# Kernel optimization log

Hardware: AMD Instinct MI355X
Metric: run time of the kernel (lower is better)

The kernel has to match this reference:

```python
import jax, jax.numpy as jnp
import numpy as np

S_GRID = 14.0
L_COORD = 5.0
L_NOOBJ = 0.5
B = 2


def _xywh2xyxy(b):
    # b: [..., 4] with (x, y, w, h); x,y are divided by S per the original module
    xy = b[..., :2] / S_GRID
    wh = b[..., 2:4]
    return jnp.concatenate([xy - 0.5 * wh, xy + 0.5 * wh], axis=-1)


def setup_inputs() -> dict:
    key = jax.random.key(0)
    k1, k2, k3, k4 = jax.random.split(key, 4)
    N, S, C = 4096, 14, 20
    pred_tensor = jax.random.uniform(k1, (N, S, S, B * 5 + C), dtype=jnp.float32, minval=0.05, maxval=1.0)
    target_boxes = jax.random.uniform(k2, (N, S, S, 4), dtype=jnp.float32, minval=0.05, maxval=1.0)
    target_cls = jax.random.normal(k3, (N, S, S, C), dtype=jnp.float32)
    has_object_map = jax.random.randint(k4, (N, S, S), 0, 2).astype(jnp.bool_)
    return {"pred_tensor": pred_tensor, "target_boxes": target_boxes,
            "target_cls": target_cls, "has_object_map": has_object_map}


def reference(pred_tensor, target_boxes, target_cls, has_object_map):
    N = pred_tensor.shape[0]
    mask = has_object_map                      # [N,S,S] bool
    maskf = mask.astype(pred_tensor.dtype)
    pb = pred_tensor[..., :B * 5].reshape(*pred_tensor.shape[:3], B, 5)  # [N,S,S,B,5]
    pc = pred_tensor[..., B * 5:]              # [N,S,S,20]

    # class loss: masked sum of squared errors over classes
    cls_loss = jnp.sum(maskf * jnp.sum((target_cls - pc) ** 2, axis=-1))

    # no-object loss: conf^2 on cells without objects, summed over both boxes
    conf = pb[..., 4]                          # [N,S,S,B]
    no_obj_loss = L_NOOBJ * jnp.sum(jnp.where(~mask[..., None], conf, 0.0) ** 2)

    # per-cell IoU of target vs each of the B predicted boxes (diag of original NxM)
    t_xyxy = _xywh2xyxy(target_boxes)          # [N,S,S,4]
    p_xyxy = _xywh2xyxy(pb[..., :4])           # [N,S,S,B,4]
    lt = jnp.maximum(t_xyxy[..., None, :2], p_xyxy[..., :2])
    rb = jnp.minimum(t_xyxy[..., None, 2:], p_xyxy[..., 2:])
    wh = jnp.clip(rb - lt, 0.0)
    inter = wh[..., 0] * wh[..., 1]            # [N,S,S,B]
    area_t = (t_xyxy[..., 2] - t_xyxy[..., 0]) * (t_xyxy[..., 3] - t_xyxy[..., 1])
    area_p = (p_xyxy[..., 2] - p_xyxy[..., 0]) * (p_xyxy[..., 3] - p_xyxy[..., 1])
    iou = inter / (area_t[..., None] + area_p - inter)  # [N,S,S,B]

    best_iou = jnp.max(iou, axis=-1)           # [N,S,S]
    best_idx = jnp.argmax(iou, axis=-1)        # [N,S,S]
    best_box = jnp.take_along_axis(pb, best_idx[..., None, None], axis=3)[..., 0, :]  # [N,S,S,5]

    xy_diff = jnp.where(mask[..., None], best_box[..., :2] - target_boxes[..., :2], 0.0)
    wh_p = jnp.where(mask[..., None], best_box[..., 2:4], 1.0)
    wh_t = jnp.where(mask[..., None], target_boxes[..., 2:4], 1.0)
    reg_loss = L_COORD * (jnp.sum(xy_diff ** 2)
                          + jnp.sum((jnp.sqrt(wh_p) - jnp.sqrt(wh_t)) ** 2))

    # containing-object confidence loss: mse(best_iou, best_box_conf) on object cells
    containing_obj_loss = jnp.sum(jnp.where(mask, best_iou - best_box[..., 4], 0.0) ** 2)

    total_loss = (cls_loss + no_obj_loss + reg_loss + containing_obj_loss) / N
    return (total_loss, reg_loss, containing_obj_loss, no_obj_loss, cls_loss)
```

## Files before the change

kernel.cpp:

```cpp
#include <hip/hip_runtime.h>
#include <math.h>


#define BLOCK 256
#define WPB 4
#define CPW 64

typedef __attribute__((address_space(3))) void       lds_void_t;
typedef __attribute__((address_space(1))) const void gbl_void_t;

__global__ __launch_bounds__(BLOCK, 4) void k_yolo(
    const float*  __restrict__ pred,
    const float4* __restrict__ tbox4,
    const float4* __restrict__ tcls4,
    const int*    __restrict__ mask,
    float4*       __restrict__ partial,
    int n_cells)
{
    __shared__ float  sp[WPB][CPW * 30];
    __shared__ float4 swr[WPB];
    const int tid  = threadIdx.x;
    const int lane = tid & 63;
    const int w    = tid >> 6;
    const long long nc    = n_cells;
    const long long cell0 = ((long long)blockIdx.x * WPB + w) * CPW;
    const long long base  = (cell0 < nc) ? cell0 : (nc - CPW);
    const int remc = (int)(((nc - base) < CPW) ? (nc - base) : CPW);
    const int lim5 = remc * 5;
    const int li   = (lane < remc) ? lane : (remc - 1);

    const char* gb   = (const char*)pred + base * 120;
    const char* gend = (const char*)pred + nc * 120 - 16;
    char* lb = (char*)&sp[w][0];
    #pragma unroll
    for (int i = 0; i < 7; ++i) {
        const char* ga = gb + i * 1024 + lane * 16;
        if (ga > gend) ga = gend;
        __builtin_amdgcn_global_load_lds((gbl_void_t*)ga,
                                         (lds_void_t*)(lb + i * 1024), 16, 0, 0);
    }
    if (lane < 32) {
        const char* ga = gb + 7168 + lane * 16;
        if (ga > gend) ga = gend;
        __builtin_amdgcn_global_load_lds((gbl_void_t*)ga,
                                         (lds_void_t*)(lb + 7168), 16, 0, 0);
    }

    int    mraw = mask[base + li];
    float4 tb   = tbox4[base + li];
    const float4* t4 = tcls4 + base * 5;
    float4 t[5];
    #pragma unroll
    for (int i = 0; i < 5; ++i) {
        int j  = lane + i * 64;
        int jc = (j < lim5) ? j : (lim5 - 1);
        t[i] = t4[jc];
    }

    __builtin_amdgcn_s_waitcnt(0xF70);
    __asm__ volatile("" ::: "memory");

    const bool  vf    = (cell0 + (long long)lane) < nc;
    const int   mflag = vf ? mraw : 0;
    const float mff   = (float)mflag;
    const float vff   = vf ? 1.0f : 0.0f;
    const unsigned long long mbits = __ballot(mflag != 0);

    float cls = 0.f, noobj, reg, cont;
    {
        const float2* pc2 = reinterpret_cast<const float2*>(sp[w] + lane * 30);
        float2 v0 = pc2[0], v1 = pc2[1], v2 = pc2[2], v3 = pc2[3], v4 = pc2[4];
        float txc = tb.x / 14.0f, tyc = tb.y / 14.0f;
        float t0 = txc - 0.5f * tb.z, t1 = tyc - 0.5f * tb.w;
        float t2 = txc + 0.5f * tb.z, t3 = tyc + 0.5f * tb.w;
        float area_t = (t2 - t0) * (t3 - t1);
        float bx[2] = { v0.x, v2.y }, by[2] = { v0.y, v3.x };
        float bw[2] = { v1.x, v3.y }, bh[2] = { v1.y, v4.x };
        float bcf[2] = { v2.x, v4.y };
        float iou[2];
        #pragma unroll
        for (int b = 0; b < 2; ++b) {
            float px = bx[b] / 14.0f, py = by[b] / 14.0f;
            float q0 = px - 0.5f * bw[b], q1 = py - 0.5f * bh[b];
            float q2 = px + 0.5f * bw[b], q3 = py + 0.5f * bh[b];
            float lt0 = fmaxf(t0, q0), lt1 = fmaxf(t1, q1);
            float rb0 = fminf(t2, q2), rb1 = fminf(t3, q3);
            float ww = fmaxf(rb0 - lt0, 0.f), hh = fmaxf(rb1 - lt1, 0.f);
            float inter = ww * hh;
            float area_p = (q2 - q0) * (q3 - q1);
            iou[b] = inter / (area_t + area_p - inter);
        }
        int bi = (iou[1] > iou[0]) ? 1 : 0;
        float dx = bx[bi] - tb.x, dy = by[bi] - tb.y;
        float swd = sqrtf(bw[bi]) - sqrtf(tb.z);
        float shd = sqrtf(bh[bi]) - sqrtf(tb.w);
        reg  = mff * 5.0f * (dx*dx + dy*dy + swd*swd + shd*shd);
        float dco = iou[bi] - bcf[bi];
        cont = mff * dco * dco;
        noobj = (vff - mff) * 0.5f * (v2.x * v2.x + v4.y * v4.y);
    }

    #pragma unroll
    for (int i = 0; i < 5; ++i) {
        int j = lane + i * 64;
        int c = j / 5;
        int q = j - 5 * c;
        float mcf = (float)((int)((mbits >> c) & 1ull));
        mcf = (j < lim5) ? mcf : 0.0f;
        const float2* s2 = reinterpret_cast<const float2*>(sp[w] + c * 30 + 10 + q * 4);
        float2 a = s2[0], b2 = s2[1];
        float d0 = t[i].x - a.x,  d1 = t[i].y - a.y;
        float d2 = t[i].z - b2.x, d3 = t[i].w - b2.y;
        cls += mcf * (d0*d0 + d1*d1 + d2*d2 + d3*d3);
    }

    #pragma unroll
    for (int off = 32; off; off >>= 1) {
        cls   += __shfl_down(cls,   off, 64);
        noobj += __shfl_down(noobj, off, 64);
        reg   += __shfl_down(reg,   off, 64);
        cont  += __shfl_down(cont,  off, 64);
    }
    if (lane == 0) swr[w] = make_float4(cls, noobj, reg, cont);
    __syncthreads();
    if (tid == 0) {
        float4 a = swr[0];
        #pragma unroll
        for (int i = 1; i < WPB; ++i) {
            float4 b = swr[i];
            a.x += b.x; a.y += b.y; a.z += b.z; a.w += b.w;
        }
        partial[blockIdx.x] = a;
    }
}

__global__ __launch_bounds__(BLOCK) void k_final(
    const float4* __restrict__ partial, int nblocks,
    float* __restrict__ out, float invN)
{
    float4 acc = make_float4(0.f, 0.f, 0.f, 0.f);
    for (int b = threadIdx.x; b < nblocks; b += BLOCK) {
        float4 v = partial[b];
        acc.x += v.x; acc.y += v.y; acc.z += v.z; acc.w += v.w;
    }
    #pragma unroll
    for (int off = 32; off; off >>= 1) {
        acc.x += __shfl_down(acc.x, off, 64);
        acc.y += __shfl_down(acc.y, off, 64);
        acc.z += __shfl_down(acc.z, off, 64);
        acc.w += __shfl_down(acc.w, off, 64);
    }
    __shared__ float4 sw[WPB];
    int lane = threadIdx.x & 63, w = threadIdx.x >> 6;
    if (lane == 0) sw[w] = acc;
    __syncthreads();
    if (threadIdx.x == 0) {
        float cls = 0.f, noobj = 0.f, reg = 0.f, cont = 0.f;
        #pragma unroll
        for (int i = 0; i < WPB; ++i) {
            cls += sw[i].x; noobj += sw[i].y; reg += sw[i].z; cont += sw[i].w;
        }
        out[0] = (cls + noobj + reg + cont) * invN;
        out[1] = reg;
        out[2] = cont;
        out[3] = noobj;
        out[4] = cls;
    }
}

extern "C" void kernel_launch(void* const* d_in, const int* in_sizes, int n_in,
                              void* d_out, int out_size, void* d_ws, size_t ws_size,
                              hipStream_t stream) {
    const float*  pred  = (const float*)d_in[0];
    const float4* tbox4 = (const float4*)d_in[1];
    const float4* tcls4 = (const float4*)d_in[2];
    const int*    mask  = (const int*)d_in[3];
    float* out = (float*)d_out;
    float4* partial = (float4*)d_ws;

    int n_cells = in_sizes[3];
    int N = in_sizes[0] / (14 * 14 * 30);
    int nblocks = (n_cells + BLOCK - 1) / BLOCK;

    hipLaunchKernelGGL(k_yolo, dim3(nblocks), dim3(BLOCK), 0, stream,
                       pred, tbox4, tcls4, mask, partial, n_cells);
    hipLaunchKernelGGL(k_final, dim3(1), dim3(BLOCK), 0, stream,
                       partial, nblocks, out, 1.0f / (float)N);
}
```

Baseline: 203.3 us.

## Process four tiles per wave with software-pipelined LDS prefetch of next tile

Each wave now loops over four 64-cell tiles instead of one, reading the current tile's prediction data from LDS into registers, then issuing the async global-to-LDS load and register loads for the next tile before computing on the current one. The aim is to overlap memory latency with compute and cut the block count and partial-sum work by a factor of four. Class-target loads use nontemporal hints. In exchange, register pressure rises from double-buffered contexts, fewer blocks are in flight, and the launch-bounds occupancy hint was dropped.

```diff
diff --git a/kernel.cpp b/kernel.cpp
--- a/kernel.cpp
+++ b/kernel.cpp
@@ -5,78 +5,98 @@
 #define BLOCK 256
 #define WPB 4
 #define CPW 64
+#define TPW 4
 
 typedef __attribute__((address_space(3))) void       lds_void_t;
 typedef __attribute__((address_space(1))) const void gbl_void_t;
-
-__global__ __launch_bounds__(BLOCK, 4) void k_yolo(
-    const float*  __restrict__ pred,
-    const float4* __restrict__ tbox4,
-    const float4* __restrict__ tcls4,
-    const int*    __restrict__ mask,
-    float4*       __restrict__ partial,
-    int n_cells)
-{
-    __shared__ float  sp[WPB][CPW * 30];
-    __shared__ float4 swr[WPB];
-    const int tid  = threadIdx.x;
-    const int lane = tid & 63;
-    const int w    = tid >> 6;
-    const long long nc    = n_cells;
-    const long long cell0 = ((long long)blockIdx.x * WPB + w) * CPW;
-    const long long base  = (cell0 < nc) ? cell0 : (nc - CPW);
-    const int remc = (int)(((nc - base) < CPW) ? (nc - base) : CPW);
-    const int lim5 = remc * 5;
-    const int li   = (lane < remc) ? lane : (remc - 1);
-
-    const char* gb   = (const char*)pred + base * 120;
+typedef float vf4 __attribute__((ext_vector_type(4)));
+
+struct TileCtx {
+    long long cell0;
+    int       lim5;
+    int       mraw;
+    vf4       tb;
+    vf4       t[5];
+};
+
+__device__ __forceinline__ void issue_tile(
+    long long tile, long long ntiles, long long nc, int lane,
+    const float* __restrict__ pred, const vf4* __restrict__ tbox4,
+    const vf4* __restrict__ tcls4, const int* __restrict__ mask,
+    char* lb, TileCtx& cx)
+{
+    cx.cell0 = tile * CPW;
+    long long tt = (tile < ntiles) ? tile : (ntiles - 1);
+    long long b  = tt * CPW;
+    b = (b + CPW <= nc) ? b : (nc - CPW);
+    int remc = (int)(((nc - b) < (long long)CPW) ? (nc - b) : CPW);
+    cx.lim5 = remc * 5;
+    int li = (lane < remc) ? lane : (remc - 1);
+
+    const char* gb   = (const char*)pred + b * 120;
     const char* gend = (const char*)pred + nc * 120 - 16;
-    char* lb = (char*)&sp[w][0];
     #pragma unroll
     for (int i = 0; i < 7; ++i) {
-        const char* ga = gb + i * 1024 + lane * 16;
+        const char* ga = gb + i * 1024 + (long long)lane * 16;
         if (ga > gend) ga = gend;
         __builtin_amdgcn_global_load_lds((gbl_void_t*)ga,
                                          (lds_void_t*)(lb + i * 1024), 16, 0, 0);
     }
     if (lane < 32) {
-        const char* ga = gb + 7168 + lane * 16;
+        const char* ga = gb + 7168 + (long long)lane * 16;
         if (ga > gend) ga = gend;
         __builtin_amdgcn_global_load_lds((gbl_void_t*)ga,
                                          (lds_void_t*)(lb + 7168), 16, 0, 0);
     }
-
-    int    mraw = mask[base + li];
-    float4 tb   = tbox4[base + li];
-    const float4* t4 = tcls4 + base * 5;
-    float4 t[5];
+    cx.mraw = mask[b + li];
+    cx.tb   = tbox4[b + li];
+    const vf4* t4 = tcls4 + b * 5;
     #pragma unroll
     for (int i = 0; i < 5; ++i) {
         int j  = lane + i * 64;
-        int jc = (j < lim5) ? j : (lim5 - 1);
-        t[i] = t4[jc];
-    }
-
-    __builtin_amdgcn_s_waitcnt(0xF70);
-    __asm__ volatile("" ::: "memory");
-
-    const bool  vf    = (cell0 + (long long)lane) < nc;
-    const int   mflag = vf ? mraw : 0;
+        int jc = (j < cx.lim5) ? j : (cx.lim5 - 1);
+        cx.t[i] = __builtin_nontemporal_load(&t4[jc]);
+    }
+}
+
+__device__ __forceinline__ void read_pred(
+    const float* spw, int lane,
+    float2 (&v)[5], float2 (&pa)[5], float2 (&pb)[5])
+{
+    const float2* pc2 = reinterpret_cast<const float2*>(spw + lane * 30);
+    #pragma unroll
+    for (int i = 0; i < 5; ++i) v[i] = pc2[i];
+    #pragma unroll
+    for (int i = 0; i < 5; ++i) {
+        int j = lane + i * 64;
+        int c = j / 5;
+        int q = j - 5 * c;
+        const float2* s2 = reinterpret_cast<const float2*>(spw + c * 30 + 10 + q * 4);
+        pa[i] = s2[0];
+        pb[i] = s2[1];
+    }
+}
+
+__device__ __forceinline__ void compute_tile(
+    int lane, long long nc, const TileCtx& cx,
+    const float2 (&v)[5], const float2 (&pa)[5], const float2 (&pb)[5],
+    float& cls, float& noobj, float& reg, float& cont)
+{
+    const bool  vfb   = (cx.cell0 + (long long)lane) < nc;
+    const int   mflag = vfb ? cx.mraw : 0;
     const float mff   = (float)mflag;
-    const float vff   = vf ? 1.0f : 0.0f;
+    const float vff   = vfb ? 1.0f : 0.0f;
     const unsigned long long mbits = __ballot(mflag != 0);
 
-    float cls = 0.f, noobj, reg, cont;
     {
-        const float2* pc2 = reinterpret_cast<const float2*>(sp[w] + lane * 30);
-        float2 v0 = pc2[0], v1 = pc2[1], v2 = pc2[2], v3 = pc2[3], v4 = pc2[4];
+        vf4 tb = cx.tb;
         float txc = tb.x / 14.0f, tyc = tb.y / 14.0f;
         float t0 = txc - 0.5f * tb.z, t1 = tyc - 0.5f * tb.w;
         float t2 = txc + 0.5f * tb.z, t3 = tyc + 0.5f * tb.w;
         float area_t = (t2 - t0) * (t3 - t1);
-        float bx[2] = { v0.x, v2.y }, by[2] = { v0.y, v3.x };
-        float bw[2] = { v1.x, v3.y }, bh[2] = { v1.y, v4.x };
-        float bcf[2] = { v2.x, v4.y };
+        float bx[2] = { v[0].x, v[2].y }, by[2] = { v[0].y, v[3].x };
+        float bw[2] = { v[1].x, v[3].y }, bh[2] = { v[1].y, v[4].x };
+        float bcf[2] = { v[2].x, v[4].y };
         float iou[2];
         #pragma unroll
         for (int b = 0; b < 2; ++b) {
@@ -94,24 +114,63 @@
         float dx = bx[bi] - tb.x, dy = by[bi] - tb.y;
         float swd = sqrtf(bw[bi]) - sqrtf(tb.z);
         float shd = sqrtf(bh[bi]) - sqrtf(tb.w);
-        reg  = mff * 5.0f * (dx*dx + dy*dy + swd*swd + shd*shd);
+        reg  += mff * 5.0f * (dx*dx + dy*dy + swd*swd + shd*shd);
         float dco = iou[bi] - bcf[bi];
-        cont = mff * dco * dco;
-        noobj = (vff - mff) * 0.5f * (v2.x * v2.x + v4.y * v4.y);
-    }
-
+        cont += mff * dco * dco;
+        noobj += (vff - mff) * 0.5f * (v[2].x * v[2].x + v[4].y * v[4].y);
+    }
     #pragma unroll
     for (int i = 0; i < 5; ++i) {
         int j = lane + i * 64;
         int c = j / 5;
-        int q = j - 5 * c;
         float mcf = (float)((int)((mbits >> c) & 1ull));
-        mcf = (j < lim5) ? mcf : 0.0f;
-        const float2* s2 = reinterpret_cast<const float2*>(sp[w] + c * 30 + 10 + q * 4);
-        float2 a = s2[0], b2 = s2[1];
-        float d0 = t[i].x - a.x,  d1 = t[i].y - a.y;
-        float d2 = t[i].z - b2.x, d3 = t[i].w - b2.y;
+        if (j >= cx.lim5) mcf = 0.0f;
+        float d0 = cx.t[i].x - pa[i].x,  d1 = cx.t[i].y - pa[i].y;
+        float d2 = cx.t[i].z - pb[i].x,  d3 = cx.t[i].w - pb[i].y;
         cls += mcf * (d0*d0 + d1*d1 + d2*d2 + d3*d3);
+    }
+}
+
+__global__ __launch_bounds__(BLOCK) void k_yolo(
+    const float* __restrict__ pred,
+    const vf4*   __restrict__ tbox4,
+    const vf4*   __restrict__ tcls4,
+    const int*   __restrict__ mask,
+    float4*      __restrict__ partial,
+    int n_cells)
+{
+    __shared__ float  sp[WPB][CPW * 30];
+    __shared__ float4 swr[WPB];
+    const int tid  = threadIdx.x;
+    const int lane = tid & 63;
+    const int w    = tid >> 6;
+    const long long nc     = n_cells;
+    const long long ntiles = (nc + CPW - 1) / CPW;
+    const long long g      = (long long)blockIdx.x * WPB + w;
+    const long long tile0  = g * TPW;
+
+    char*        lb  = (char*)&sp[w][0];
+    const float* spw = &sp[w][0];
+
+    float cls = 0.f, noobj = 0.f, reg = 0.f, cont = 0.f;
+    float2 v[5], pa[5], pb[5];
+    TileCtx cx[2];
+
+    issue_tile(tile0, ntiles, nc, lane, pred, tbox4, tcls4, mask, lb, cx[0]);
+    #pragma unroll
+    for (int s = 0; s < TPW; ++s) {
+        __builtin_amdgcn_s_waitcnt(0x0F70);
+        __asm__ volatile("" ::: "memory");
+        read_pred(spw, lane, v, pa, pb);
+        __builtin_amdgcn_s_waitcnt(0xC07F);
+        __asm__ volatile("" ::: "memory");
+        __builtin_amdgcn_sched_barrier(0);
+        if (s + 1 < TPW)
+            issue_tile(tile0 + s + 1, ntiles, nc, lane,
+                       pred, tbox4, tcls4, mask, lb, cx[(s + 1) & 1]);
+        __builtin_amdgcn_sched_barrier(0);
+        compute_tile(lane, nc, cx[s & 1], v, pa, pb,
+                     cls, noobj, reg, cont);
     }
 
     #pragma unroll
@@ -134,14 +193,14 @@
     }
 }
 
-__global__ __launch_bounds__(BLOCK) void k_final(
+__global__ __launch_bounds__(256) void k_final(
     const float4* __restrict__ partial, int nblocks,
     float* __restrict__ out, float invN)
 {
     float4 acc = make_float4(0.f, 0.f, 0.f, 0.f);
-    for (int b = threadIdx.x; b < nblocks; b += BLOCK) {
-        float4 v = partial[b];
-        acc.x += v.x; acc.y += v.y; acc.z += v.z; acc.w += v.w;
+    for (int b = threadIdx.x; b < nblocks; b += 256) {
+        float4 p = partial[b];
+        acc.x += p.x; acc.y += p.y; acc.z += p.z; acc.w += p.w;
     }
     #pragma unroll
     for (int off = 32; off; off >>= 1) {
@@ -150,14 +209,14 @@
         acc.z += __shfl_down(acc.z, off, 64);
         acc.w += __shfl_down(acc.w, off, 64);
     }
-    __shared__ float4 sw[WPB];
+    __shared__ float4 sw[4];
     int lane = threadIdx.x & 63, w = threadIdx.x >> 6;
     if (lane == 0) sw[w] = acc;
     __syncthreads();
     if (threadIdx.x == 0) {
         float cls = 0.f, noobj = 0.f, reg = 0.f, cont = 0.f;
         #pragma unroll
-        for (int i = 0; i < WPB; ++i) {
+        for (int i = 0; i < 4; ++i) {
             cls += sw[i].x; noobj += sw[i].y; reg += sw[i].z; cont += sw[i].w;
         }
         out[0] = (cls + noobj + reg + cont) * invN;
@@ -171,19 +230,21 @@
 extern "C" void kernel_launch(void* const* d_in, const int* in_sizes, int n_in,
                               void* d_out, int out_size, void* d_ws, size_t ws_size,
                               hipStream_t stream) {
-    const float*  pred  = (const float*)d_in[0];
-    const float4* tbox4 = (const float4*)d_in[1];
-    const float4* tcls4 = (const float4*)d_in[2];
-    const int*    mask  = (const int*)d_in[3];
+    const float* pred  = (const float*)d_in[0];
+    const vf4*   tbox4 = (const vf4*)d_in[1];
+    const vf4*   tcls4 = (const vf4*)d_in[2];
+    const int*   mask  = (const int*)d_in[3];
     float* out = (float*)d_out;
     float4* partial = (float4*)d_ws;
 
     int n_cells = in_sizes[3];
     int N = in_sizes[0] / (14 * 14 * 30);
-    int nblocks = (n_cells + BLOCK - 1) / BLOCK;
+    long long ntiles  = (n_cells + CPW - 1) / CPW;
+    long long nwaves  = (ntiles + TPW - 1) / TPW;
+    int nblocks = (int)((nwaves + WPB - 1) / WPB);
 
     hipLaunchKernelGGL(k_yolo, dim3(nblocks), dim3(BLOCK), 0, stream,
                        pred, tbox4, tcls4, mask, partial, n_cells);
-    hipLaunchKernelGGL(k_final, dim3(1), dim3(BLOCK), 0, stream,
+    hipLaunchKernelGGL(k_final, dim3(1), dim3(256), 0, stream,
                        partial, nblocks, out, 1.0f / (float)N);
 }
```

After: 202.1 us. Within noise of the previous version (-0.6%).
